# Kernel optimization log

Hardware: AMD Instinct MI355X
Metric: run time of the kernel (lower is better)

Reference implementation:

```python
import jax, jax.numpy as jnp
import numpy as np

B, C, N, K, COUT = 8, 128, 10000, 16, 256


def setup_inputs() -> dict:
    key = jax.random.key(0)
    ks = jax.random.split(key, 8)
    x = jax.random.normal(ks[0], (B, C, N, 1), dtype=jnp.float32)
    edge_index = jax.random.randint(ks[1], (2, B, N, K), 0, N)
    s1 = 1.0 / np.sqrt(C)
    W1 = jax.random.uniform(ks[2], (C, C), jnp.float32, -s1, s1)   # nn1 1x1 conv weight
    b1 = jax.random.uniform(ks[3], (C,), jnp.float32, -s1, s1)
    Wp = jax.random.uniform(ks[4], (C, C), jnp.float32, -s1, s1)   # nn_pooling Linear
    bp = jax.random.uniform(ks[5], (C,), jnp.float32, -s1, s1)
    s2 = 1.0 / np.sqrt(2 * C)
    W2 = jax.random.uniform(ks[6], (COUT, 2 * C), jnp.float32, -s2, s2)  # nn2 1x1 conv
    b2 = jax.random.uniform(ks[7], (COUT,), jnp.float32, -s2, s2)
    return dict(x=x, edge_index=edge_index, W1=W1, b1=b1, Wp=Wp, bp=bp, W2=W2, b2=b2)


def reference(x, edge_index, W1, b1, Wp, bp, W2, b2):
    b, c, n, _ = x.shape
    k = edge_index.shape[-1]
    # nn1: 1x1 conv (channel mix) + ReLU -> [B,C,N,1]
    h = jax.nn.relu(jnp.einsum('bcns,dc->bdns', x, W1) + b1[None, :, None, None])
    # batched_index_select: gather neighbor features along vertex dim -> [B,C,N,K]
    hn = h[:, :, :, 0]                              # [B,C,N]
    idx = edge_index[0].reshape(b, 1, n * k)        # broadcast over C
    xj = jnp.take_along_axis(hn, idx, axis=2).reshape(b, c, n, k)
    # nn_pooling: Linear over channel dim + ReLU (transpose(1,3) in torch == act on C)
    xj = jax.nn.relu(jnp.einsum('bcnk,dc->bdnk', xj, Wp) + bp[None, :, None, None])
    # max-pool over neighbors, keepdim -> [B,C,N,1]
    xj = jnp.max(xj, axis=-1, keepdims=True)
    # concat along channels, nn2: 1x1 conv + ReLU -> [B,COUT,N,1]
    cat = jnp.concatenate([h, xj], axis=1)
    out = jax.nn.relu(jnp.einsum('bcns,dc->bdns', cat, W2) + b2[None, :, None, None])
    return out
```

## Files before the change

kernel.cpp:

```cpp
#include <hip/hip_runtime.h>

#define NODES 10000
#define BATCH 8
#define CH    128
#define KNB   16
#define CO    256

typedef __bf16 bf16x8 __attribute__((ext_vector_type(8)));
typedef float  f32x4  __attribute__((ext_vector_type(4)));

__device__ __forceinline__ unsigned short f2bf(float f) {
  unsigned u = __float_as_uint(f);
  u = (u + 0x7FFFu + ((u >> 16) & 1u)) >> 16;
  return (unsigned short)u;
}
__device__ __forceinline__ unsigned pk2(float a, float b) {
  return (unsigned)f2bf(a) | ((unsigned)f2bf(b) << 16);
}
__device__ __forceinline__ unsigned pkmax(unsigned a, unsigned b) {
  unsigned d;
  asm("v_pk_max_u16 %0, %1, %2" : "=v"(d) : "v"(a), "v"(b));
  return d;
}
__device__ __forceinline__ uint4 pkmax4(uint4 a, uint4 b) {
  a.x = pkmax(a.x, b.x); a.y = pkmax(a.y, b.y);
  a.z = pkmax(a.z, b.z); a.w = pkmax(a.w, b.w);
  return a;
}
__device__ __forceinline__ bf16x8 asbf8(uint4 u) {
  union { uint4 u; bf16x8 b; } c; c.u = u; return c.b;
}

__global__ __launch_bounds__(256) void prep(
    const float* __restrict__ W1, const float* __restrict__ Wp,
    const float* __restrict__ W2,
    unsigned short* __restrict__ W1b, unsigned short* __restrict__ Wpb,
    unsigned short* __restrict__ W2b)
{
  int i = blockIdx.x * 256 + threadIdx.x;
  const float* src; unsigned short* dst; int off;
  if (i < 4096)      { src = W1; dst = W1b; off = i; }
  else if (i < 8192) { src = Wp; dst = Wpb; off = i - 4096; }
  else               { src = W2; dst = W2b; off = i - 8192; }
  float4 v = ((const float4*)src)[off];
  ushort4 o;
  o.x = f2bf(v.x); o.y = f2bf(v.y); o.z = f2bf(v.z); o.w = f2bf(v.w);
  ((ushort4*)dst)[off] = o;
}

__global__ __launch_bounds__(256) void fused_hz(
    const unsigned short* __restrict__ W1b, const float* __restrict__ b1,
    const unsigned short* __restrict__ Wpb, const float* __restrict__ bp,
    const float* __restrict__ x,
    unsigned short* __restrict__ h_t, unsigned short* __restrict__ z_t)
{
  const int b    = blockIdx.y;
  const int t    = threadIdx.x;
  const int w    = t >> 6, lane = t & 63;
  const int lm   = lane & 15, q = lane >> 4;
  const int nw0  = blockIdx.x * 64 + w * 16;

  __shared__ __align__(16) unsigned short Hs_all[4][16 * 128];
  char* Hs = (char*)Hs_all[w];

  const int node = nw0 + lm;
  const int gn   = (node < NODES) ? node : (NODES - 1);

  const float* X = x + (size_t)b * CH * NODES + gn;
  float xv[4][8];
#pragma unroll
  for (int kt = 0; kt < 4; ++kt)
#pragma unroll
    for (int j = 0; j < 8; ++j)
      xv[kt][j] = X[(size_t)(kt * 32 + q * 8 + j) * NODES];

  uint4 B1[4];
#pragma unroll
  for (int kt = 0; kt < 4; ++kt) {
    B1[kt].x = pk2(xv[kt][0], xv[kt][1]);
    B1[kt].y = pk2(xv[kt][2], xv[kt][3]);
    B1[kt].z = pk2(xv[kt][4], xv[kt][5]);
    B1[kt].w = pk2(xv[kt][6], xv[kt][7]);
  }

  uint4 a_cur[4], a_nxt[4];
#pragma unroll
  for (int kt = 0; kt < 4; ++kt)
    a_cur[kt] = *(const uint4*)(W1b + (size_t)(lm) * CH + kt * 32 + q * 8);

#pragma unroll
  for (int dt = 0; dt < 8; ++dt) {
    if (dt < 7) {
#pragma unroll
      for (int kt = 0; kt < 4; ++kt)
        a_nxt[kt] = *(const uint4*)(W1b + (size_t)((dt + 1) * 16 + lm) * CH
                                    + kt * 32 + q * 8);
    }
    f32x4 acc = (f32x4){0.f, 0.f, 0.f, 0.f};
#pragma unroll
    for (int kt = 0; kt < 4; ++kt)
      acc = __builtin_amdgcn_mfma_f32_16x16x32_bf16(
          asbf8(a_cur[kt]), asbf8(B1[kt]), acc, 0, 0, 0);

    const int d0 = dt * 16 + q * 4;
    float4 bi = *(const float4*)(b1 + d0);
    ushort4 o;
    o.x = f2bf(fmaxf(acc[0] + bi.x, 0.f));
    o.y = f2bf(fmaxf(acc[1] + bi.y, 0.f));
    o.z = f2bf(fmaxf(acc[2] + bi.z, 0.f));
    o.w = f2bf(fmaxf(acc[3] + bi.w, 0.f));
    if (node < NODES)
      *(ushort4*)(h_t + ((size_t)b * NODES + node) * CH + d0) = o;
    const int chunk = dt * 2 + (q >> 1);
    *(ushort4*)(Hs + lm * 256 + ((chunk ^ (lm & 7)) << 4) + ((q & 1) << 3)) = o;
#pragma unroll
    for (int kt = 0; kt < 4; ++kt) a_cur[kt] = a_nxt[kt];
  }

  uint4 B2[4];
#pragma unroll
  for (int kt = 0; kt < 4; ++kt)
    B2[kt] = *(const uint4*)(Hs + lm * 256 + (((kt * 4 + q) ^ (lm & 7)) << 4));

#pragma unroll
  for (int kt = 0; kt < 4; ++kt)
    a_cur[kt] = *(const uint4*)(Wpb + (size_t)(lm) * CH + kt * 32 + q * 8);

#pragma unroll
  for (int dt = 0; dt < 8; ++dt) {
    if (dt < 7) {
#pragma unroll
      for (int kt = 0; kt < 4; ++kt)
        a_nxt[kt] = *(const uint4*)(Wpb + (size_t)((dt + 1) * 16 + lm) * CH
                                    + kt * 32 + q * 8);
    }
    f32x4 acc = (f32x4){0.f, 0.f, 0.f, 0.f};
#pragma unroll
    for (int kt = 0; kt < 4; ++kt)
      acc = __builtin_amdgcn_mfma_f32_16x16x32_bf16(
          asbf8(a_cur[kt]), asbf8(B2[kt]), acc, 0, 0, 0);

    const int d0 = dt * 16 + q * 4;
    float4 bi = *(const float4*)(bp + d0);
    if (node < NODES) {
      ushort4 o;
      o.x = f2bf(fmaxf(acc[0] + bi.x, 0.f));
      o.y = f2bf(fmaxf(acc[1] + bi.y, 0.f));
      o.z = f2bf(fmaxf(acc[2] + bi.z, 0.f));
      o.w = f2bf(fmaxf(acc[3] + bi.w, 0.f));
      *(ushort4*)(z_t + ((size_t)b * NODES + node) * CH + d0) = o;
    }
#pragma unroll
    for (int kt = 0; kt < 4; ++kt) a_cur[kt] = a_nxt[kt];
  }
}

__global__ __launch_bounds__(128) void out_kernel(
    const unsigned short* __restrict__ h_t, const unsigned short* __restrict__ z_t,
    const int* __restrict__ e0, const unsigned short* __restrict__ W2b,
    const float* __restrict__ b2, float* __restrict__ out)
{
  const int bid = blockIdx.x;
  const int b   = bid & 7;
  const int t   = threadIdx.x;
  const int w   = t >> 6, lane = t & 63;
  const int nw0 = (bid >> 3) * 64 + w * 32;

  __shared__ __align__(16) unsigned short cat_all[2][32 * 256];
  char* cat = (char*)cat_all[w];

  const int nl4 = lane >> 2, c = lane & 3;
  const char* Zb = (const char*)z_t + (size_t)b * NODES * (CH * 2);
#pragma unroll
  for (int p = 0; p < 2; ++p) {
    const int nl = p * 16 + nl4;
    int gn = nw0 + nl; if (gn >= NODES) gn = NODES - 1;

    const char* H = (const char*)h_t + ((size_t)b * NODES + gn) * (CH * 2);
    uint4 hv[4];
#pragma unroll
    for (int j = 0; j < 4; ++j)
      hv[j] = *(const uint4*)(H + ((4 * j + c) << 4));

    const int* ep = e0 + ((size_t)b * NODES + gn) * KNB;
    unsigned idxv[KNB];
#pragma unroll
    for (int jq = 0; jq < 4; ++jq) {
      uint4 iv = *(const uint4*)(ep + jq * 4);
      idxv[jq * 4 + 0] = iv.x; idxv[jq * 4 + 1] = iv.y;
      idxv[jq * 4 + 2] = iv.z; idxv[jq * 4 + 3] = iv.w;
    }

    uint4 m[4];
#pragma unroll
    for (int j = 0; j < 4; ++j) m[j] = make_uint4(0u, 0u, 0u, 0u);
#pragma unroll
    for (int k = 0; k < KNB; ++k) {
      const char* pz = Zb + (size_t)idxv[k] * (CH * 2);
#pragma unroll
      for (int j = 0; j < 4; ++j)
        m[j] = pkmax4(m[j], *(const uint4*)(pz + ((4 * j + c) << 4)));
    }

#pragma unroll
    for (int j = 0; j < 4; ++j) {
      const int ch = 4 * j + c;
      *(uint4*)(cat + nl * 512 + ((ch ^ (nl & 7)) << 4)) = hv[j];
      const int cz = 16 + 4 * j + c;
      *(uint4*)(cat + nl * 512 + ((cz ^ (nl & 7)) << 4)) = m[j];
    }
  }

  const int lm = lane & 15, q = lane >> 4;
  uint4 Bf[2][8];
#pragma unroll
  for (int nt = 0; nt < 2; ++nt)
#pragma unroll
    for (int kt = 0; kt < 8; ++kt)
      Bf[nt][kt] = *(const uint4*)(cat + (nt * 16 + lm) * 512
                                   + (((kt * 4 + q) ^ (lm & 7)) << 4));

  uint4 a_cur[4], a_nxt[4];
#pragma unroll
  for (int kt = 0; kt < 4; ++kt)
    a_cur[kt] = *(const uint4*)(W2b + (size_t)lm * CO + kt * 32 + q * 8);

  f32x4 acc0 = (f32x4){0.f, 0.f, 0.f, 0.f};
  f32x4 acc1 = (f32x4){0.f, 0.f, 0.f, 0.f};

#pragma unroll
  for (int s = 0; s < 32; ++s) {
    const int dt = s >> 1, half = s & 1;
    if (s < 31) {
      const int dn = (s + 1) >> 1, hn = (s + 1) & 1;
#pragma unroll
      for (int kt = 0; kt < 4; ++kt)
        a_nxt[kt] = *(const uint4*)(W2b + (size_t)(dn * 16 + lm) * CO
                                    + (hn * 4 + kt) * 32 + q * 8);
    }
#pragma unroll
    for (int kt = 0; kt < 4; ++kt) {
      const int ktg = half * 4 + kt;
      acc0 = __builtin_amdgcn_mfma_f32_16x16x32_bf16(
          asbf8(a_cur[kt]), asbf8(Bf[0][ktg]), acc0, 0, 0, 0);
      acc1 = __builtin_amdgcn_mfma_f32_16x16x32_bf16(
          asbf8(a_cur[kt]), asbf8(Bf[1][ktg]), acc1, 0, 0, 0);
    }
    if (half == 1) {
      const int d0 = dt * 16 + q * 4;
      float4 bi = *(const float4*)(b2 + d0);
      float bv[4] = {bi.x, bi.y, bi.z, bi.w};
      f32x4 aa[2] = {acc0, acc1};
#pragma unroll
      for (int nt = 0; nt < 2; ++nt) {
        const int gn = nw0 + nt * 16 + lm;
        if (gn < NODES) {
          float* op = out + (size_t)(b * CO + d0) * NODES + gn;
#pragma unroll
          for (int r = 0; r < 4; ++r)
            op[(size_t)r * NODES] = fmaxf(aa[nt][r] + bv[r], 0.f);
        }
      }
      acc0 = (f32x4){0.f, 0.f, 0.f, 0.f};
      acc1 = (f32x4){0.f, 0.f, 0.f, 0.f};
    }
#pragma unroll
    for (int kt = 0; kt < 4; ++kt) a_cur[kt] = a_nxt[kt];
  }
}

extern "C" void kernel_launch(void* const* d_in, const int* in_sizes, int n_in,
                              void* d_out, int out_size, void* d_ws, size_t ws_size,
                              hipStream_t stream) {
  const float* x  = (const float*)d_in[0];
  const int*   ei = (const int*)d_in[1];
  const float* W1 = (const float*)d_in[2];
  const float* b1 = (const float*)d_in[3];
  const float* Wp = (const float*)d_in[4];
  const float* bp = (const float*)d_in[5];
  const float* W2 = (const float*)d_in[6];
  const float* b2 = (const float*)d_in[7];
  float* out = (float*)d_out;

  unsigned short* ws  = (unsigned short*)d_ws;
  unsigned short* h_t = ws;
  unsigned short* z_t = h_t + (size_t)BATCH * NODES * CH;
  unsigned short* W1b = z_t + (size_t)BATCH * NODES * CH;
  unsigned short* Wpb = W1b + CH * CH;
  unsigned short* W2b = Wpb + CH * CH;

  prep<<<96, 256, 0, stream>>>(W1, Wp, W2, W1b, Wpb, W2b);

  const int NT = (NODES + 63) / 64;
  fused_hz<<<dim3(NT, BATCH), 256, 0, stream>>>(W1b, b1, Wpb, bp, x, h_t, z_t);
  out_kernel<<<BATCH * NT, 128, 0, stream>>>(h_t, z_t, ei, W2b, b2, out);
}
```

Measured before the change: 230.9 us.

## Double node tiles per wave and load MFMA fragments directly, dropping LDS staging

```diff
diff --git a/kernel.cpp b/kernel.cpp
--- a/kernel.cpp
+++ b/kernel.cpp
@@ -58,104 +58,124 @@
   const int t    = threadIdx.x;
   const int w    = t >> 6, lane = t & 63;
   const int lm   = lane & 15, q = lane >> 4;
-  const int nw0  = blockIdx.x * 64 + w * 16;
-
-  __shared__ __align__(16) unsigned short Hs_all[4][16 * 128];
+  const int nw0  = blockIdx.x * 128 + w * 32;
+
+  __shared__ __align__(16) unsigned short Hs_all[4][32 * 128];
   char* Hs = (char*)Hs_all[w];
 
-  const int node = nw0 + lm;
-  const int gn   = (node < NODES) ? node : (NODES - 1);
-
-  const float* X = x + (size_t)b * CH * NODES + gn;
-  float xv[4][8];
-#pragma unroll
-  for (int kt = 0; kt < 4; ++kt)
-#pragma unroll
-    for (int j = 0; j < 8; ++j)
-      xv[kt][j] = X[(size_t)(kt * 32 + q * 8 + j) * NODES];
-
-  uint4 B1[4];
+  int node[2], gn[2];
+  node[0] = nw0 + lm;      gn[0] = node[0] < NODES ? node[0] : NODES - 1;
+  node[1] = nw0 + 16 + lm; gn[1] = node[1] < NODES ? node[1] : NODES - 1;
+
+  uint4 B1[2][4];
+#pragma unroll
+  for (int nt = 0; nt < 2; ++nt) {
+    const float* X = x + (size_t)b * CH * NODES + gn[nt];
+    float xv[32];
+#pragma unroll
+    for (int kt = 0; kt < 4; ++kt)
+#pragma unroll
+      for (int j = 0; j < 8; ++j)
+        xv[kt * 8 + j] = X[(size_t)(kt * 32 + q * 8 + j) * NODES];
+#pragma unroll
+    for (int kt = 0; kt < 4; ++kt) {
+      B1[nt][kt].x = pk2(xv[kt * 8 + 0], xv[kt * 8 + 1]);
+      B1[nt][kt].y = pk2(xv[kt * 8 + 2], xv[kt * 8 + 3]);
+      B1[nt][kt].z = pk2(xv[kt * 8 + 4], xv[kt * 8 + 5]);
+      B1[nt][kt].w = pk2(xv[kt * 8 + 6], xv[kt * 8 + 7]);
+    }
+  }
+
+  uint4 a[2][4];
 #pragma unroll
   for (int kt = 0; kt < 4; ++kt) {
-    B1[kt].x = pk2(xv[kt][0], xv[kt][1]);
-    B1[kt].y = pk2(xv[kt][2], xv[kt][3]);
-    B1[kt].z = pk2(xv[kt][4], xv[kt][5]);
-    B1[kt].w = pk2(xv[kt][6], xv[kt][7]);
-  }
-
-  uint4 a_cur[4], a_nxt[4];
-#pragma unroll
-  for (int kt = 0; kt < 4; ++kt)
-    a_cur[kt] = *(const uint4*)(W1b + (size_t)(lm) * CH + kt * 32 + q * 8);
-
+    a[0][kt] = *(const uint4*)(W1b + (size_t)(0 * 16 + lm) * CH + kt * 32 + q * 8);
+    a[1][kt] = *(const uint4*)(W1b + (size_t)(1 * 16 + lm) * CH + kt * 32 + q * 8);
+  }
 #pragma unroll
   for (int dt = 0; dt < 8; ++dt) {
-    if (dt < 7) {
+    f32x4 acc0 = (f32x4){0.f, 0.f, 0.f, 0.f};
+    f32x4 acc1 = (f32x4){0.f, 0.f, 0.f, 0.f};
+#pragma unroll
+    for (int kt = 0; kt < 4; ++kt) {
+      acc0 = __builtin_amdgcn_mfma_f32_16x16x32_bf16(
+          asbf8(a[dt & 1][kt]), asbf8(B1[0][kt]), acc0, 0, 0, 0);
+      acc1 = __builtin_amdgcn_mfma_f32_16x16x32_bf16(
+          asbf8(a[dt & 1][kt]), asbf8(B1[1][kt]), acc1, 0, 0, 0);
+    }
+    if (dt < 6) {
 #pragma unroll
       for (int kt = 0; kt < 4; ++kt)
-        a_nxt[kt] = *(const uint4*)(W1b + (size_t)((dt + 1) * 16 + lm) * CH
-                                    + kt * 32 + q * 8);
-    }
-    f32x4 acc = (f32x4){0.f, 0.f, 0.f, 0.f};
-#pragma unroll
-    for (int kt = 0; kt < 4; ++kt)
-      acc = __builtin_amdgcn_mfma_f32_16x16x32_bf16(
-          asbf8(a_cur[kt]), asbf8(B1[kt]), acc, 0, 0, 0);
-
+        a[dt & 1][kt] = *(const uint4*)(W1b + (size_t)((dt + 2) * 16 + lm) * CH
+                                        + kt * 32 + q * 8);
+    }
     const int d0 = dt * 16 + q * 4;
     float4 bi = *(const float4*)(b1 + d0);
-    ushort4 o;
-    o.x = f2bf(fmaxf(acc[0] + bi.x, 0.f));
-    o.y = f2bf(fmaxf(acc[1] + bi.y, 0.f));
-    o.z = f2bf(fmaxf(acc[2] + bi.z, 0.f));
-    o.w = f2bf(fmaxf(acc[3] + bi.w, 0.f));
-    if (node < NODES)
-      *(ushort4*)(h_t + ((size_t)b * NODES + node) * CH + d0) = o;
-    const int chunk = dt * 2 + (q >> 1);
-    *(ushort4*)(Hs + lm * 256 + ((chunk ^ (lm & 7)) << 4) + ((q & 1) << 3)) = o;
-#pragma unroll
-    for (int kt = 0; kt < 4; ++kt) a_cur[kt] = a_nxt[kt];
-  }
-
-  uint4 B2[4];
-#pragma unroll
-  for (int kt = 0; kt < 4; ++kt)
-    B2[kt] = *(const uint4*)(Hs + lm * 256 + (((kt * 4 + q) ^ (lm & 7)) << 4));
-
-#pragma unroll
-  for (int kt = 0; kt < 4; ++kt)
-    a_cur[kt] = *(const uint4*)(Wpb + (size_t)(lm) * CH + kt * 32 + q * 8);
-
+    f32x4 aa[2] = {acc0, acc1};
+#pragma unroll
+    for (int nt = 0; nt < 2; ++nt) {
+      ushort4 o;
+      o.x = f2bf(fmaxf(aa[nt][0] + bi.x, 0.f));
+      o.y = f2bf(fmaxf(aa[nt][1] + bi.y, 0.f));
+      o.z = f2bf(fmaxf(aa[nt][2] + bi.z, 0.f));
+      o.w = f2bf(fmaxf(aa[nt][3] + bi.w, 0.f));
+      if (node[nt] < NODES)
+        *(ushort4*)(h_t + ((size_t)b * NODES + node[nt]) * CH + d0) = o;
+      const int row = nt * 16 + lm;
+      const int chunk = dt * 2 + (q >> 1);
+      *(ushort4*)(Hs + row * 256 + ((chunk ^ (row & 7)) << 4) + ((q & 1) << 3)) = o;
+    }
+  }
+
+  uint4 B2[2][4];
+#pragma unroll
+  for (int nt = 0; nt < 2; ++nt) {
+    const int row = nt * 16 + lm;
+#pragma unroll
+    for (int kt = 0; kt < 4; ++kt)
+      B2[nt][kt] = *(const uint4*)(Hs + row * 256 + (((kt * 4 + q) ^ (row & 7)) << 4));
+  }
+
+#pragma unroll
+  for (int kt = 0; kt < 4; ++kt) {
+    a[0][kt] = *(const uint4*)(Wpb + (size_t)(0 * 16 + lm) * CH + kt * 32 + q * 8);
+    a[1][kt] = *(const uint4*)(Wpb + (size_t)(1 * 16 + lm) * CH + kt * 32 + q * 8);
+  }
 #pragma unroll
   for (int dt = 0; dt < 8; ++dt) {
-    if (dt < 7) {
+    f32x4 acc0 = (f32x4){0.f, 0.f, 0.f, 0.f};
+    f32x4 acc1 = (f32x4){0.f, 0.f, 0.f, 0.f};
+#pragma unroll
+    for (int kt = 0; kt < 4; ++kt) {
+      acc0 = __builtin_amdgcn_mfma_f32_16x16x32_bf16(
+          asbf8(a[dt & 1][kt]), asbf8(B2[0][kt]), acc0, 0, 0, 0);
+      acc1 = __builtin_amdgcn_mfma_f32_16x16x32_bf16(
+          asbf8(a[dt & 1][kt]), asbf8(B2[1][kt]), acc1, 0, 0, 0);
+    }
+    if (dt < 6) {
 #pragma unroll
       for (int kt = 0; kt < 4; ++kt)
-        a_nxt[kt] = *(const uint4*)(Wpb + (size_t)((dt + 1) * 16 + lm) * CH
-                                    + kt * 32 + q * 8);
-    }
-    f32x4 acc = (f32x4){0.f, 0.f, 0.f, 0.f};
-#pragma unroll
-    for (int kt = 0; kt < 4; ++kt)
-      acc = __builtin_amdgcn_mfma_f32_16x16x32_bf16(
-          asbf8(a_cur[kt]), asbf8(B2[kt]), acc, 0, 0, 0);
-
+        a[dt & 1][kt] = *(const uint4*)(Wpb + (size_t)((dt + 2) * 16 + lm) * CH
+                                        + kt * 32 + q * 8);
+    }
     const int d0 = dt * 16 + q * 4;
     float4 bi = *(const float4*)(bp + d0);
-    if (node < NODES) {
-      ushort4 o;
-      o.x = f2bf(fmaxf(acc[0] + bi.x, 0.f));
-      o.y = f2bf(fmaxf(acc[1] + bi.y, 0.f));
-      o.z = f2bf(fmaxf(acc[2] + bi.z, 0.f));
-      o.w = f2bf(fmaxf(acc[3] + bi.w, 0.f));
-      *(ushort4*)(z_t + ((size_t)b * NODES + node) * CH + d0) = o;
-    }
-#pragma unroll
-    for (int kt = 0; kt < 4; ++kt) a_cur[kt] = a_nxt[kt];
-  }
-}
-
-__global__ __launch_bounds__(128) void out_kernel(
+    f32x4 aa[2] = {acc0, acc1};
+#pragma unroll
+    for (int nt = 0; nt < 2; ++nt) {
+      if (node[nt] < NODES) {
+        ushort4 o;
+        o.x = f2bf(fmaxf(aa[nt][0] + bi.x, 0.f));
+        o.y = f2bf(fmaxf(aa[nt][1] + bi.y, 0.f));
+        o.z = f2bf(fmaxf(aa[nt][2] + bi.z, 0.f));
+        o.w = f2bf(fmaxf(aa[nt][3] + bi.w, 0.f));
+        *(ushort4*)(z_t + ((size_t)b * NODES + node[nt]) * CH + d0) = o;
+      }
+    }
+  }
+}
+
+__global__ __launch_bounds__(256) void out_kernel(
     const unsigned short* __restrict__ h_t, const unsigned short* __restrict__ z_t,
     const int* __restrict__ e0, const unsigned short* __restrict__ W2b,
     const float* __restrict__ b2, float* __restrict__ out)
@@ -164,87 +184,79 @@
   const int b   = bid & 7;
   const int t   = threadIdx.x;
   const int w   = t >> 6, lane = t & 63;
-  const int nw0 = (bid >> 3) * 64 + w * 32;
-
-  __shared__ __align__(16) unsigned short cat_all[2][32 * 256];
-  char* cat = (char*)cat_all[w];
-
-  const int nl4 = lane >> 2, c = lane & 3;
-  const char* Zb = (const char*)z_t + (size_t)b * NODES * (CH * 2);
-#pragma unroll
-  for (int p = 0; p < 2; ++p) {
-    const int nl = p * 16 + nl4;
-    int gn = nw0 + nl; if (gn >= NODES) gn = NODES - 1;
-
-    const char* H = (const char*)h_t + ((size_t)b * NODES + gn) * (CH * 2);
-    uint4 hv[4];
-#pragma unroll
-    for (int j = 0; j < 4; ++j)
-      hv[j] = *(const uint4*)(H + ((4 * j + c) << 4));
-
-    const int* ep = e0 + ((size_t)b * NODES + gn) * KNB;
-    unsigned idxv[KNB];
+  const int lm  = lane & 15, q = lane >> 4;
+  const int nw0 = (bid >> 3) * 128 + w * 32;
+
+  int node[2], gn[2];
+  node[0] = nw0 + lm;      gn[0] = node[0] < NODES ? node[0] : NODES - 1;
+  node[1] = nw0 + 16 + lm; gn[1] = node[1] < NODES ? node[1] : NODES - 1;
+
+  uint4 iv[2][4];
+#pragma unroll
+  for (int nt = 0; nt < 2; ++nt)
+#pragma unroll
+    for (int jq = 0; jq < 4; ++jq)
+      iv[nt][jq] = *(const uint4*)(e0 + ((size_t)b * NODES + gn[nt]) * KNB + jq * 4);
+
+  uint4 Bf[2][8];
+#pragma unroll
+  for (int nt = 0; nt < 2; ++nt)
+#pragma unroll
+    for (int kt = 0; kt < 4; ++kt)
+      Bf[nt][kt] = *(const uint4*)(h_t + ((size_t)b * NODES + gn[nt]) * CH
+                                   + (kt * 4 + q) * 8);
+
+  const unsigned short* Zb = z_t + (size_t)b * NODES * CH;
+#pragma unroll
+  for (int nt = 0; nt < 2; ++nt) {
+    unsigned jns[KNB];
 #pragma unroll
     for (int jq = 0; jq < 4; ++jq) {
-      uint4 iv = *(const uint4*)(ep + jq * 4);
-      idxv[jq * 4 + 0] = iv.x; idxv[jq * 4 + 1] = iv.y;
-      idxv[jq * 4 + 2] = iv.z; idxv[jq * 4 + 3] = iv.w;
-    }
-
+      jns[jq * 4 + 0] = iv[nt][jq].x; jns[jq * 4 + 1] = iv[nt][jq].y;
+      jns[jq * 4 + 2] = iv[nt][jq].z; jns[jq * 4 + 3] = iv[nt][jq].w;
+    }
     uint4 m[4];
 #pragma unroll
     for (int j = 0; j < 4; ++j) m[j] = make_uint4(0u, 0u, 0u, 0u);
 #pragma unroll
     for (int k = 0; k < KNB; ++k) {
-      const char* pz = Zb + (size_t)idxv[k] * (CH * 2);
+      const unsigned short* pz = Zb + (size_t)jns[k] * CH + q * 8;
 #pragma unroll
       for (int j = 0; j < 4; ++j)
-        m[j] = pkmax4(m[j], *(const uint4*)(pz + ((4 * j + c) << 4)));
-    }
-
-#pragma unroll
-    for (int j = 0; j < 4; ++j) {
-      const int ch = 4 * j + c;
-      *(uint4*)(cat + nl * 512 + ((ch ^ (nl & 7)) << 4)) = hv[j];
-      const int cz = 16 + 4 * j + c;
-      *(uint4*)(cat + nl * 512 + ((cz ^ (nl & 7)) << 4)) = m[j];
-    }
-  }
-
-  const int lm = lane & 15, q = lane >> 4;
-  uint4 Bf[2][8];
-#pragma unroll
-  for (int nt = 0; nt < 2; ++nt)
-#pragma unroll
-    for (int kt = 0; kt < 8; ++kt)
-      Bf[nt][kt] = *(const uint4*)(cat + (nt * 16 + lm) * 512
-                                   + (((kt * 4 + q) ^ (lm & 7)) << 4));
-
-  uint4 a_cur[4], a_nxt[4];
-#pragma unroll
-  for (int kt = 0; kt < 4; ++kt)
-    a_cur[kt] = *(const uint4*)(W2b + (size_t)lm * CO + kt * 32 + q * 8);
+        m[j] = pkmax4(m[j], *(const uint4*)(pz + j * 32));
+    }
+#pragma unroll
+    for (int j = 0; j < 4; ++j) Bf[nt][4 + j] = m[j];
+  }
+
+  uint4 A[3][4];
+#pragma unroll
+  for (int s = 0; s < 3; ++s)
+#pragma unroll
+    for (int kt = 0; kt < 4; ++kt)
+      A[s][kt] = *(const uint4*)(W2b + (size_t)((s >> 1) * 16 + lm) * CO
+                                 + ((s & 1) * 4 + kt) * 32 + q * 8);
 
   f32x4 acc0 = (f32x4){0.f, 0.f, 0.f, 0.f};
   f32x4 acc1 = (f32x4){0.f, 0.f, 0.f, 0.f};
 
 #pragma unroll
   for (int s = 0; s < 32; ++s) {
-    const int dt = s >> 1, half = s & 1;
-    if (s < 31) {
-      const int dn = (s + 1) >> 1, hn = (s + 1) & 1;
-#pragma unroll
-      for (int kt = 0; kt < 4; ++kt)
-        a_nxt[kt] = *(const uint4*)(W2b + (size_t)(dn * 16 + lm) * CO
-                                    + (hn * 4 + kt) * 32 + q * 8);
-    }
+    const int dt = s >> 1, half = s & 1, slot = s % 3;
 #pragma unroll
     for (int kt = 0; kt < 4; ++kt) {
       const int ktg = half * 4 + kt;
       acc0 = __builtin_amdgcn_mfma_f32_16x16x32_bf16(
-          asbf8(a_cur[kt]), asbf8(Bf[0][ktg]), acc0, 0, 0, 0);
+          asbf8(A[slot][kt]), asbf8(Bf[0][ktg]), acc0, 0, 0, 0);
       acc1 = __builtin_amdgcn_mfma_f32_16x16x32_bf16(
-          asbf8(a_cur[kt]), asbf8(Bf[1][ktg]), acc1, 0, 0, 0);
+          asbf8(A[slot][kt]), asbf8(Bf[1][ktg]), acc1, 0, 0, 0);
+    }
+    if (s + 3 < 32) {
+      const int sn = s + 3, dn = sn >> 1, hn = sn & 1;
+#pragma unroll
+      for (int kt = 0; kt < 4; ++kt)
+        A[slot][kt] = *(const uint4*)(W2b + (size_t)(dn * 16 + lm) * CO
+                                      + (hn * 4 + kt) * 32 + q * 8);
     }
     if (half == 1) {
       const int d0 = dt * 16 + q * 4;
@@ -253,9 +265,8 @@
       f32x4 aa[2] = {acc0, acc1};
 #pragma unroll
       for (int nt = 0; nt < 2; ++nt) {
-        const int gn = nw0 + nt * 16 + lm;
-        if (gn < NODES) {
-          float* op = out + (size_t)(b * CO + d0) * NODES + gn;
+        if (node[nt] < NODES) {
+          float* op = out + (size_t)(b * CO + d0) * NODES + node[nt];
 #pragma unroll
           for (int r = 0; r < 4; ++r)
             op[(size_t)r * NODES] = fmaxf(aa[nt][r] + bv[r], 0.f);
@@ -264,8 +275,6 @@
       acc0 = (f32x4){0.f, 0.f, 0.f, 0.f};
       acc1 = (f32x4){0.f, 0.f, 0.f, 0.f};
     }
-#pragma unroll
-    for (int kt = 0; kt < 4; ++kt) a_cur[kt] = a_nxt[kt];
   }
 }
 
@@ -291,7 +300,7 @@
 
   prep<<<96, 256, 0, stream>>>(W1, Wp, W2, W1b, Wpb, W2b);
 
-  const int NT = (NODES + 63) / 64;
+  const int NT = (NODES + 127) / 128;
   fused_hz<<<dim3(NT, BATCH), 256, 0, stream>>>(W1b, b1, Wpb, bp, x, h_t, z_t);
-  out_kernel<<<BATCH * NT, 128, 0, stream>>>(h_t, z_t, ei, W2b, b2, out);
-}
+  out_kernel<<<BATCH * NT, 256, 0, stream>>>(h_t, z_t, ei, W2b, b2, out);
+}
```

New measurement: 249.4 us. +8.0%, slower.
